# Optimization experiments

Hardware: AMD Instinct MI355X
Metric: run time of the kernel (lower is better)

Reference implementation:

```python
import jax, jax.numpy as jnp
import numpy as np

SIZE = 512
FEATURES = 16
IN_FEATURES = 16
BATCH = 8192
EXCLUSIVE = 1  # module init arg exclusive=True


def setup_inputs() -> dict:
    key = jax.random.key(0)
    k1, k2, k3, k4 = jax.random.split(key, 4)
    inputs = jax.random.normal(k1, (BATCH, IN_FEATURES), dtype=jnp.float32)
    cache = jax.random.normal(k2, (BATCH, SIZE, IN_FEATURES), dtype=jnp.float32)
    kernel = jax.random.normal(k3, (SIZE * IN_FEATURES, SIZE * FEATURES), dtype=jnp.float32)
    bias = jax.random.normal(k4, (SIZE, FEATURES), dtype=jnp.float32)
    index = 300
    return {"inputs": inputs, "cache": cache, "kernel": kernel, "bias": bias, "index": index}


def reference(inputs, cache, kernel, bias, index):
    # Faithful translation of FastMaskedDense1D.update_site.
    batch, in_features = inputs.shape
    size, features = bias.shape
    size_i = index + 1

    # scatter the new input site into the cache (index - exclusive >= 0 branch)
    if index - EXCLUSIVE >= 0:
        cache = cache.at[:, index - EXCLUSIVE, :].set(inputs)

    # cached inputs up to the current site, flattened: (batch, size_i*in_features)
    cache_i = cache[:, :size_i, :].reshape(batch, size_i * in_features)

    # dynamic slice of the kernel for output site `index`: (size_i, in_features, features)
    kernel_i = kernel.reshape(size, in_features, size, features)[:size_i, :, index, :]

    # triu(ones, exclusive) kron ones mask, sliced at [:size_i, :, index, :]:
    # row j is 1 iff index >= j + exclusive
    mask = (jnp.arange(size_i) <= index - EXCLUSIVE).astype(kernel_i.dtype)
    kernel_i = (kernel_i * mask[:, None, None]).reshape(size_i * in_features, features)

    y_i = cache_i @ kernel_i + bias[index, :]  # (batch, features)
    return y_i
```

## Files before the change

### kernel.cpp

```cpp
#include <hip/hip_runtime.h>


#define EXCLUSIVE 1
#define SIZEV     512
#define NF        16
#define NIF       16
#define KROW      (SIZEV * NF)
#define CROW      (SIZEV * NIF)
#define MB        16
#define KCH       256
#define SK        20
#define NW        8

__device__ __forceinline__ void fma4(float4& a, float s, float4 b) {
    a.x = fmaf(s, b.x, a.x);
    a.y = fmaf(s, b.y, a.y);
    a.z = fmaf(s, b.z, a.z);
    a.w = fmaf(s, b.w, a.w);
}

__device__ __forceinline__ float4 red4(float4 v, int m) {
    v.x += __shfl_xor(v.x, m, 64);
    v.y += __shfl_xor(v.y, m, 64);
    v.z += __shfl_xor(v.z, m, 64);
    v.w += __shfl_xor(v.w, m, 64);
    return v;
}

__global__ __launch_bounds__(256) void pack_k(
    const float* __restrict__ kern,
    const int*   __restrict__ idxp,
    float*       __restrict__ kp)
{
    const int index = *idxp;
    const int jc = index - EXCLUSIVE + 1;
    const int KT = (jc > 0) ? jc * NIF : 0;
    const int KTpad = (KT + KCH - 1) & ~(KCH - 1);
    const int t  = blockIdx.x * blockDim.x + threadIdx.x;
    const int r  = t >> 2;
    const int q  = t & 3;
    if (r < KTpad) {
        float4 v = {0.f, 0.f, 0.f, 0.f};
        if (r < KT)
            v = *(const float4*)(kern + (size_t)r * KROW + (size_t)index * NF + 4 * q);
        *(float4*)(kp + (size_t)r * NF + 4 * q) = v;
    }
}

__global__ __launch_bounds__(512, 4) void fmd_kernel(
    const float* __restrict__ inputs,
    const float* __restrict__ cache,
    const float* __restrict__ kp,
    const float* __restrict__ bias,
    const int*   __restrict__ idxp,
    float*       __restrict__ out)
{
    __shared__ float Kl[2][KCH * SK];
    __shared__ float Red[NW * MB * NF];

    const int index = *idxp;
    const int jc = index - EXCLUSIVE + 1;
    const int KM = (jc > 0) ? (jc - 1) * NIF : 0;
    const int NC = (KM + KCH - 1) / KCH;

    const int tid  = threadIdx.x;
    const int lane = tid & 63;
    const int ks   = tid >> 6;
    const int kq   = lane & 15;
    const int rq   = lane >> 4;
    const int row0 = blockIdx.x * MB;

    const int srow = tid >> 1;
    const int sq   = (tid & 1) * 2;

    float4 acc[4][4];
    #pragma unroll
    for (int r = 0; r < 4; ++r)
        #pragma unroll
        for (int q = 0; q < 4; ++q)
            acc[r][q] = make_float4(0.f, 0.f, 0.f, 0.f);

    const float4* kpv = (const float4*)kp;
    const float* Abase = cache + (size_t)(row0 + rq * 4) * CROW + kq + 16 * ks;

    float4 st0, st1;
    float  aR[2][4], aN[2][4];

    if (NC > 0) {
        st0 = kpv[(size_t)4 * srow + sq];
        st1 = kpv[(size_t)4 * srow + sq + 1];
        *(float4*)&Kl[0][srow * SK + 4 * sq]       = st0;
        *(float4*)&Kl[0][srow * SK + 4 * (sq + 1)] = st1;
        #pragma unroll
        for (int t = 0; t < 2; ++t)
            #pragma unroll
            for (int r = 0; r < 4; ++r)
                aR[t][r] = Abase[(size_t)r * CROW + 128 * t];

        for (int c = 0; c < NC; ++c) {
            const int k0 = c * KCH;
            if (c + 1 < NC) {
                const int kn = k0 + KCH;
                st0 = kpv[(size_t)4 * (kn + srow) + sq];
                st1 = kpv[(size_t)4 * (kn + srow) + sq + 1];
                #pragma unroll
                for (int t = 0; t < 2; ++t)
                    #pragma unroll
                    for (int r = 0; r < 4; ++r)
                        aN[t][r] = Abase[(size_t)r * CROW + kn + 128 * t];
            }
            __syncthreads();

            const int buf  = c & 1;
            const int kend = min(KCH, KM - k0);
            const float* Kb = &Kl[buf][0];

            #pragma unroll
            for (int t = 0; t < 2; ++t) {
                const int sb = 16 * ks + 128 * t;
                if (sb < kend) {
                    const float* Kp = Kb + (kq + sb) * SK;
                    float4 kv0 = *(const float4*)(Kp);
                    float4 kv1 = *(const float4*)(Kp + 4);
                    float4 kv2 = *(const float4*)(Kp + 8);
                    float4 kv3 = *(const float4*)(Kp + 12);
                    #pragma unroll
                    for (int r = 0; r < 4; ++r) {
                        const float a = aR[t][r];
                        fma4(acc[r][0], a, kv0);
                        fma4(acc[r][1], a, kv1);
                        fma4(acc[r][2], a, kv2);
                        fma4(acc[r][3], a, kv3);
                    }
                }
            }

            if (c + 1 < NC) {
                const int b2 = (c + 1) & 1;
                *(float4*)&Kl[b2][srow * SK + 4 * sq]       = st0;
                *(float4*)&Kl[b2][srow * SK + 4 * (sq + 1)] = st1;
                #pragma unroll
                for (int t = 0; t < 2; ++t)
                    #pragma unroll
                    for (int r = 0; r < 4; ++r)
                        aR[t][r] = aN[t][r];
            }
        }
    }

    if (jc > 0 && ks == 0) {
        const float* kg = kp + (size_t)((jc - 1) * NIF + kq) * NF;
        float4 kv0 = *(const float4*)(kg);
        float4 kv1 = *(const float4*)(kg + 4);
        float4 kv2 = *(const float4*)(kg + 8);
        float4 kv3 = *(const float4*)(kg + 12);
        #pragma unroll
        for (int r = 0; r < 4; ++r) {
            const float a = inputs[(size_t)(row0 + rq * 4 + r) * NIF + kq];
            fma4(acc[r][0], a, kv0);
            fma4(acc[r][1], a, kv1);
            fma4(acc[r][2], a, kv2);
            fma4(acc[r][3], a, kv3);
        }
    }

    #pragma unroll
    for (int m = 1; m <= 8; m <<= 1)
        #pragma unroll
        for (int r = 0; r < 4; ++r)
            #pragma unroll
            for (int q = 0; q < 4; ++q)
                acc[r][q] = red4(acc[r][q], m);

    float4 v = acc[0][0];
    #pragma unroll
    for (int r = 0; r < 4; ++r)
        #pragma unroll
        for (int q = 0; q < 4; ++q)
            if ((kq >> 2) == r && (kq & 3) == q) v = acc[r][q];
    {
        const int row  = rq * 4 + (kq >> 2);
        const int quad = kq & 3;
        *(float4*)&Red[ks * (MB * NF) + row * NF + 4 * quad] = v;
    }
    __syncthreads();

    if (tid < MB * NF) {
        const int f = tid & 15;
        float s = bias[(size_t)index * NF + f];
        #pragma unroll
        for (int ww = 0; ww < NW; ++ww)
            s += Red[ww * (MB * NF) + tid];
        out[(size_t)row0 * NF + tid] = s;
    }
}

extern "C" void kernel_launch(void* const* d_in, const int* in_sizes, int n_in,
                              void* d_out, int out_size, void* d_ws, size_t ws_size,
                              hipStream_t stream) {
    const float* inputs = (const float*)d_in[0];
    const float* cache  = (const float*)d_in[1];
    const float* kern   = (const float*)d_in[2];
    const float* bias   = (const float*)d_in[3];
    const int*   idxp   = (const int*)d_in[4];
    float*       out    = (float*)d_out;
    float*       kp     = (float*)d_ws;

    const int batch = in_sizes[0] / NIF;
    const int grid  = batch / MB;

    pack_k<<<(SIZEV * NIF * 4) / 256, 256, 0, stream>>>(kern, idxp, kp);
    fmd_kernel<<<grid, 512, 0, stream>>>(inputs, cache, kp, bias, idxp, out);
}
```

Before: 442.9 us.

## Transpose packed kernel slice and read it from global memory without LDS staging

The packed kernel slice is now stored transposed (feature-major), so each thread can load float4 runs along K directly from global/L1 instead of staging through double-buffered LDS with barriers. Blocks shrink to 256 threads and 8 rows, and each lane handles 4 consecutive K elements with float4 cache loads and prefetch. This removes LDS traffic and per-chunk synchronisation, at the cost of repeated global reads of the small kernel slice, more registers, and a twice-as-large grid.

Measured after the change: 464.3 us. 1.05x slower.

```diff
diff --git a/kernel.cpp b/kernel.cpp
--- a/kernel.cpp
+++ b/kernel.cpp
@@ -7,17 +7,9 @@
 #define NIF       16
 #define KROW      (SIZEV * NF)
 #define CROW      (SIZEV * NIF)
-#define MB        16
-#define KCH       256
-#define SK        20
-#define NW        8
-
-__device__ __forceinline__ void fma4(float4& a, float s, float4 b) {
-    a.x = fmaf(s, b.x, a.x);
-    a.y = fmaf(s, b.y, a.y);
-    a.z = fmaf(s, b.z, a.z);
-    a.w = fmaf(s, b.w, a.w);
-}
+#define MB        8
+#define NW        4
+#define KP        8192
 
 __device__ __forceinline__ float4 red4(float4 v, int m) {
     v.x += __shfl_xor(v.x, m, 64);
@@ -27,41 +19,39 @@
     return v;
 }
 
-__global__ __launch_bounds__(256) void pack_k(
+__global__ __launch_bounds__(256) void pack_kt(
     const float* __restrict__ kern,
     const int*   __restrict__ idxp,
-    float*       __restrict__ kp)
+    float*       __restrict__ kpT)
 {
     const int index = *idxp;
     const int jc = index - EXCLUSIVE + 1;
     const int KT = (jc > 0) ? jc * NIF : 0;
-    const int KTpad = (KT + KCH - 1) & ~(KCH - 1);
-    const int t  = blockIdx.x * blockDim.x + threadIdx.x;
-    const int r  = t >> 2;
-    const int q  = t & 3;
+    const int KTpad = (KT + 255) & ~255;
+    const int t = blockIdx.x * blockDim.x + threadIdx.x;
+    const int r = t >> 4;
+    const int f = t & 15;
     if (r < KTpad) {
-        float4 v = {0.f, 0.f, 0.f, 0.f};
+        float v = 0.f;
         if (r < KT)
-            v = *(const float4*)(kern + (size_t)r * KROW + (size_t)index * NF + 4 * q);
-        *(float4*)(kp + (size_t)r * NF + 4 * q) = v;
-    }
-}
-
-__global__ __launch_bounds__(512, 4) void fmd_kernel(
+            v = kern[(size_t)r * KROW + (size_t)index * NF + f];
+        kpT[(size_t)f * KP + r] = v;
+    }
+}
+
+__global__ __launch_bounds__(256, 4) void fmd_kernel(
     const float* __restrict__ inputs,
     const float* __restrict__ cache,
-    const float* __restrict__ kp,
+    const float* __restrict__ kpT,
     const float* __restrict__ bias,
     const int*   __restrict__ idxp,
     float*       __restrict__ out)
 {
-    __shared__ float Kl[2][KCH * SK];
     __shared__ float Red[NW * MB * NF];
 
     const int index = *idxp;
     const int jc = index - EXCLUSIVE + 1;
     const int KM = (jc > 0) ? (jc - 1) * NIF : 0;
-    const int NC = (KM + KCH - 1) / KCH;
 
     const int tid  = threadIdx.x;
     const int lane = tid & 63;
@@ -70,118 +60,114 @@
     const int rq   = lane >> 4;
     const int row0 = blockIdx.x * MB;
 
-    const int srow = tid >> 1;
-    const int sq   = (tid & 1) * 2;
-
-    float4 acc[4][4];
+    float acc[2][16];
     #pragma unroll
-    for (int r = 0; r < 4; ++r)
-        #pragma unroll
-        for (int q = 0; q < 4; ++q)
-            acc[r][q] = make_float4(0.f, 0.f, 0.f, 0.f);
-
-    const float4* kpv = (const float4*)kp;
-    const float* Abase = cache + (size_t)(row0 + rq * 4) * CROW + kq + 16 * ks;
-
-    float4 st0, st1;
-    float  aR[2][4], aN[2][4];
-
-    if (NC > 0) {
-        st0 = kpv[(size_t)4 * srow + sq];
-        st1 = kpv[(size_t)4 * srow + sq + 1];
-        *(float4*)&Kl[0][srow * SK + 4 * sq]       = st0;
-        *(float4*)&Kl[0][srow * SK + 4 * (sq + 1)] = st1;
-        #pragma unroll
-        for (int t = 0; t < 2; ++t)
-            #pragma unroll
-            for (int r = 0; r < 4; ++r)
-                aR[t][r] = Abase[(size_t)r * CROW + 128 * t];
-
-        for (int c = 0; c < NC; ++c) {
-            const int k0 = c * KCH;
-            if (c + 1 < NC) {
-                const int kn = k0 + KCH;
-                st0 = kpv[(size_t)4 * (kn + srow) + sq];
-                st1 = kpv[(size_t)4 * (kn + srow) + sq + 1];
-                #pragma unroll
-                for (int t = 0; t < 2; ++t)
-                    #pragma unroll
-                    for (int r = 0; r < 4; ++r)
-                        aN[t][r] = Abase[(size_t)r * CROW + kn + 128 * t];
+    for (int r = 0; r < 2; ++r)
+        #pragma unroll
+        for (int f = 0; f < 16; ++f)
+            acc[r][f] = 0.f;
+
+    const float* Abase = cache + (size_t)(row0 + rq * 2) * CROW + 4 * kq;
+
+    float4 aR[2], aN[2];
+    int k0 = 64 * ks;
+
+    if (k0 < KM) {
+        #pragma unroll
+        for (int r = 0; r < 2; ++r)
+            aR[r] = *(const float4*)(Abase + (size_t)r * CROW + k0);
+
+        for (; k0 < KM; k0 += 4 * 64) {
+            const int kn = k0 + 4 * 64;
+            if (kn < KM) {
+                #pragma unroll
+                for (int r = 0; r < 2; ++r)
+                    aN[r] = *(const float4*)(Abase + (size_t)r * CROW + kn);
             }
-            __syncthreads();
-
-            const int buf  = c & 1;
-            const int kend = min(KCH, KM - k0);
-            const float* Kb = &Kl[buf][0];
-
-            #pragma unroll
-            for (int t = 0; t < 2; ++t) {
-                const int sb = 16 * ks + 128 * t;
-                if (sb < kend) {
-                    const float* Kp = Kb + (kq + sb) * SK;
-                    float4 kv0 = *(const float4*)(Kp);
-                    float4 kv1 = *(const float4*)(Kp + 4);
-                    float4 kv2 = *(const float4*)(Kp + 8);
-                    float4 kv3 = *(const float4*)(Kp + 12);
-                    #pragma unroll
-                    for (int r = 0; r < 4; ++r) {
-                        const float a = aR[t][r];
-                        fma4(acc[r][0], a, kv0);
-                        fma4(acc[r][1], a, kv1);
-                        fma4(acc[r][2], a, kv2);
-                        fma4(acc[r][3], a, kv3);
+
+            float4 aC[2];
+            aC[0] = aR[0]; aC[1] = aR[1];
+            const int nv = KM - k0;
+            if (nv < 64) {
+                const int rem = nv - 4 * kq;
+                #pragma unroll
+                for (int r = 0; r < 2; ++r) {
+                    if (rem <= 0) { aC[r].x = 0.f; aC[r].y = 0.f; aC[r].z = 0.f; aC[r].w = 0.f; }
+                    else {
+                        if (rem < 2) aC[r].y = 0.f;
+                        if (rem < 3) aC[r].z = 0.f;
+                        if (rem < 4) aC[r].w = 0.f;
                     }
                 }
             }
 
-            if (c + 1 < NC) {
-                const int b2 = (c + 1) & 1;
-                *(float4*)&Kl[b2][srow * SK + 4 * sq]       = st0;
-                *(float4*)&Kl[b2][srow * SK + 4 * (sq + 1)] = st1;
-                #pragma unroll
-                for (int t = 0; t < 2; ++t)
+            #pragma unroll
+            for (int h = 0; h < 2; ++h) {
+                float4 kT[8];
+                #pragma unroll
+                for (int fi = 0; fi < 8; ++fi)
+                    kT[fi] = *(const float4*)&kpT[(size_t)(8 * h + fi) * KP + k0 + 4 * kq];
+                #pragma unroll
+                for (int r = 0; r < 2; ++r) {
                     #pragma unroll
-                    for (int r = 0; r < 4; ++r)
-                        aR[t][r] = aN[t][r];
+                    for (int fi = 0; fi < 8; ++fi) {
+                        const int f = 8 * h + fi;
+                        acc[r][f] = fmaf(aC[r].x, kT[fi].x, acc[r][f]);
+                        acc[r][f] = fmaf(aC[r].y, kT[fi].y, acc[r][f]);
+                        acc[r][f] = fmaf(aC[r].z, kT[fi].z, acc[r][f]);
+                        acc[r][f] = fmaf(aC[r].w, kT[fi].w, acc[r][f]);
+                    }
+                }
             }
+
+            if (kn < KM) { aR[0] = aN[0]; aR[1] = aN[1]; }
         }
     }
 
     if (jc > 0 && ks == 0) {
-        const float* kg = kp + (size_t)((jc - 1) * NIF + kq) * NF;
-        float4 kv0 = *(const float4*)(kg);
-        float4 kv1 = *(const float4*)(kg + 4);
-        float4 kv2 = *(const float4*)(kg + 8);
-        float4 kv3 = *(const float4*)(kg + 12);
-        #pragma unroll
-        for (int r = 0; r < 4; ++r) {
-            const float a = inputs[(size_t)(row0 + rq * 4 + r) * NIF + kq];
-            fma4(acc[r][0], a, kv0);
-            fma4(acc[r][1], a, kv1);
-            fma4(acc[r][2], a, kv2);
-            fma4(acc[r][3], a, kv3);
+        const int kr = (jc - 1) * NIF + kq;
+        float kv[16];
+        #pragma unroll
+        for (int f = 0; f < 16; ++f)
+            kv[f] = kpT[(size_t)f * KP + kr];
+        #pragma unroll
+        for (int r = 0; r < 2; ++r) {
+            const float a = inputs[(size_t)(row0 + rq * 2 + r) * NIF + kq];
+            #pragma unroll
+            for (int f = 0; f < 16; ++f)
+                acc[r][f] = fmaf(a, kv[f], acc[r][f]);
         }
     }
 
     #pragma unroll
-    for (int m = 1; m <= 8; m <<= 1)
-        #pragma unroll
-        for (int r = 0; r < 4; ++r)
+    for (int m = 1; m <= 8; m <<= 1) {
+        #pragma unroll
+        for (int r = 0; r < 2; ++r) {
+            float4 v0 = make_float4(acc[r][0],  acc[r][1],  acc[r][2],  acc[r][3]);
+            float4 v1 = make_float4(acc[r][4],  acc[r][5],  acc[r][6],  acc[r][7]);
+            float4 v2 = make_float4(acc[r][8],  acc[r][9],  acc[r][10], acc[r][11]);
+            float4 v3 = make_float4(acc[r][12], acc[r][13], acc[r][14], acc[r][15]);
+            v0 = red4(v0, m); v1 = red4(v1, m); v2 = red4(v2, m); v3 = red4(v3, m);
+            acc[r][0]=v0.x;  acc[r][1]=v0.y;  acc[r][2]=v0.z;  acc[r][3]=v0.w;
+            acc[r][4]=v1.x;  acc[r][5]=v1.y;  acc[r][6]=v1.z;  acc[r][7]=v1.w;
+            acc[r][8]=v2.x;  acc[r][9]=v2.y;  acc[r][10]=v2.z; acc[r][11]=v2.w;
+            acc[r][12]=v3.x; acc[r][13]=v3.y; acc[r][14]=v3.z; acc[r][15]=v3.w;
+        }
+    }
+
+    if (kq < 8) {
+        const int r = kq & 1;
+        const int q = kq >> 1;
+        float4 v = make_float4(0.f, 0.f, 0.f, 0.f);
+        #pragma unroll
+        for (int rr = 0; rr < 2; ++rr)
             #pragma unroll
-            for (int q = 0; q < 4; ++q)
-                acc[r][q] = red4(acc[r][q], m);
-
-    float4 v = acc[0][0];
-    #pragma unroll
-    for (int r = 0; r < 4; ++r)
-        #pragma unroll
-        for (int q = 0; q < 4; ++q)
-            if ((kq >> 2) == r && (kq & 3) == q) v = acc[r][q];
-    {
-        const int row  = rq * 4 + (kq >> 2);
-        const int quad = kq & 3;
-        *(float4*)&Red[ks * (MB * NF) + row * NF + 4 * quad] = v;
+            for (int qq = 0; qq < 4; ++qq)
+                if (rr == r && qq == q)
+                    v = make_float4(acc[rr][4*qq], acc[rr][4*qq+1],
+                                    acc[rr][4*qq+2], acc[rr][4*qq+3]);
+        const int row = rq * 2 + r;
+        *(float4*)&Red[ks * (MB * NF) + row * NF + 4 * q] = v;
     }
     __syncthreads();
 
@@ -204,11 +190,11 @@
     const float* bias   = (const float*)d_in[3];
     const int*   idxp   = (const int*)d_in[4];
     float*       out    = (float*)d_out;
-    float*       kp     = (float*)d_ws;
+    float*       kpT    = (float*)d_ws;
 
     const int batch = in_sizes[0] / NIF;
     const int grid  = batch / MB;
 
-    pack_k<<<(SIZEV * NIF * 4) / 256, 256, 0, stream>>>(kern, idxp, kp);
-    fmd_kernel<<<grid, 512, 0, stream>>>(inputs, cache, kp, bias, idxp, out);
-}
+    pack_kt<<<(SIZEV * NIF * NF) / 256, 256, 0, stream>>>(kern, idxp, kpT);
+    fmd_kernel<<<grid, 256, 0, stream>>>(inputs, cache, kpT, bias, idxp, out);
+}
```
